# Kernel optimization log

Measured on AMD Instinct MI355X. Metric: run time of the kernel, lower is better.

The kernel has to match this reference:

```python
import jax, jax.numpy as jnp
import numpy as np


def segment_softmax(x, seg, num_segments):
    # numerically-stable softmax over graph segments (rows of the sparse matrix)
    m = jax.ops.segment_max(x, seg, num_segments=num_segments)
    e = jnp.exp(x - m[seg])
    s = jax.ops.segment_sum(e, seg, num_segments=num_segments)
    return e / s[seg]


def setup_inputs() -> dict:
    key = jax.random.key(0)
    ks = jax.random.split(key, 12)
    B, N, E, P, H = 256, 51200, 102400, 5, 300
    instruction = jax.random.normal(ks[0], (B, H), dtype=jnp.float32)
    distribution = jax.random.uniform(ks[1], (N,), dtype=jnp.float32)
    node_attrs = jax.random.normal(ks[2], (N, H), dtype=jnp.float32)
    edge_attrs = jax.random.normal(ks[3], (E, H), dtype=jnp.float32)
    node_indices = jnp.sort(jax.random.randint(ks[4], (N,), 0, B)).astype(jnp.int32)
    edge_batch_indices = jax.random.randint(ks[5], (E,), 0, B).astype(jnp.int32)
    edge_indices = jax.random.randint(ks[6], (2, E), 0, N).astype(jnp.int32)
    prop_embeds = jax.random.normal(ks[7], (P, H), dtype=jnp.float32)
    Ws_property = jax.random.uniform(ks[8], (P, H, H), dtype=jnp.float32)
    W_state = jax.random.uniform(ks[9], (H,), dtype=jnp.float32)
    W_relation = jax.random.uniform(ks[10], (H,), dtype=jnp.float32)
    return {"instruction": instruction, "distribution": distribution, "node_attrs": node_attrs,
            "edge_attrs": edge_attrs, "node_indices": node_indices,
            "edge_batch_indices": edge_batch_indices, "edge_indices": edge_indices,
            "prop_embeds": prop_embeds, "Ws_property": Ws_property,
            "W_state": W_state, "W_relation": W_relation}


def reference(instruction, distribution, node_attrs, edge_attrs, node_indices,
              edge_batch_indices, edge_indices, prop_embeds, Ws_property,
              W_state, W_relation):
    B = instruction.shape[0]
    # [B, P] property similarities
    prop_sim = jax.nn.softmax(instruction @ prop_embeds.T, axis=1)
    ps_node = prop_sim[node_indices]            # [N, P]
    instr_node = instruction[node_indices]      # [N, H]
    # per-property transform of node attrs: [N, P-1, H]
    wx = jnp.einsum('phk,nk->nph', Ws_property[:-1], node_attrs)
    node_scores = jax.nn.elu(jnp.sum(ps_node[:, :-1, None] * instr_node[:, None, :] * wx, axis=1))  # [N, H]
    # relation transform of edge attrs: [E, H]
    edge_wx = jnp.einsum('hk,ek->eh', Ws_property[-1], edge_attrs)
    edge_scores = jax.nn.elu(instruction[edge_batch_indices] * edge_wx)  # [E, H]
    # per-graph (segment) softmax over state logits
    state_logits = node_scores @ W_state        # [N]
    next_states = segment_softmax(state_logits, node_indices, B)
    # scatter-add message passing: dst node accumulates distribution[src] * edge_scores
    agg = jnp.zeros_like(node_scores).at[edge_indices[1]].add(
        distribution[edge_indices[0], None] * edge_scores)  # [N, H]
    rel_logits = agg @ W_relation               # [N]
    next_relations = segment_softmax(rel_logits, node_indices, B)
    r = ps_node[:, -1]
    next_distribution = r * next_relations + (1.0 - r) * next_states
    return next_distribution, prop_sim
```

## Files before the change

### kernel.cpp

```cpp
#include <hip/hip_runtime.h>
#include <math.h>

#define H 300
#define PP 5
#define NE 128
#define KC 32
#define NCH 10
#define ROWB 128
#define WTILE (320 * ROWB)
#define WHALF (160 * ROWB)
#define ATILE (NE * ROWB)
#define NTHREADS 256
#define GT 512

using short8 = __attribute__((ext_vector_type(8))) short;
using f32x4  = __attribute__((ext_vector_type(4))) float;

__device__ __forceinline__ float wsum64(float v) {
#pragma unroll
    for (int m = 32; m >= 1; m >>= 1) v += __shfl_xor(v, m, 64);
    return v;
}
__device__ __forceinline__ float wmax64(float v) {
#pragma unroll
    for (int m = 32; m >= 1; m >>= 1) v = fmaxf(v, __shfl_xor(v, m, 64));
    return v;
}
__device__ __forceinline__ float eluf(float x) { return x > 0.f ? x : expm1f(x); }

__device__ __forceinline__ unsigned short f2bf(float x) {
    unsigned int u = __float_as_uint(x);
    unsigned int r = u + 0x7FFF + ((u >> 16) & 1);
    return (unsigned short)(r >> 16);
}
__device__ __forceinline__ float bf2f(unsigned short h) {
    return __uint_as_float(((unsigned int)h) << 16);
}
__device__ __forceinline__ int sw(int r, int kb) {
    return r * ROWB + (kb ^ ((r & 7) << 4));
}
__device__ __forceinline__ void split4(const float* v, uint2& ph, uint2& pl) {
    unsigned short hs[4], ls[4];
#pragma unroll
    for (int i = 0; i < 4; ++i) {
        hs[i] = f2bf(v[i]);
        ls[i] = f2bf(v[i] - bf2f(hs[i]));
    }
    ph = make_uint2((unsigned)hs[0] | ((unsigned)hs[1] << 16),
                    (unsigned)hs[2] | ((unsigned)hs[3] << 16));
    pl = make_uint2((unsigned)ls[0] | ((unsigned)ls[1] << 16),
                    (unsigned)ls[2] | ((unsigned)ls[3] << 16));
}
__device__ __forceinline__ void gload16(const void* g, void* lds) {
    __builtin_amdgcn_global_load_lds(
        (const __attribute__((address_space(1))) unsigned int*)g,
        (__attribute__((address_space(3))) unsigned int*)lds, 16, 0, 0);
}
#define SBAR() __builtin_amdgcn_s_barrier()
#define SCHED() __builtin_amdgcn_sched_barrier(0)
#define WAIT_LGKM() asm volatile("s_waitcnt lgkmcnt(0)" ::: "memory")
#define WAIT_VM0()  asm volatile("s_waitcnt vmcnt(0)" ::: "memory")
#define WAIT_VM4()  asm volatile("s_waitcnt vmcnt(4)" ::: "memory")
#define WAIT_VM5()  asm volatile("s_waitcnt vmcnt(5)" ::: "memory")

__global__ void k_prop_sim(const float* __restrict__ instr,
                           const float* __restrict__ pe,
                           float* __restrict__ prop_sim) {
    int b = blockIdx.x, lane = threadIdx.x;
    float dots[PP];
#pragma unroll
    for (int p = 0; p < PP; ++p) {
        float s = 0.f;
        for (int hh = lane; hh < H; hh += 64) s += instr[b * H + hh] * pe[p * H + hh];
        dots[p] = wsum64(s);
    }
    if (lane == 0) {
        float m = dots[0];
#pragma unroll
        for (int p = 1; p < PP; ++p) m = fmaxf(m, dots[p]);
        float e[PP], s = 0.f;
#pragma unroll
        for (int p = 0; p < PP; ++p) { e[p] = expf(dots[p] - m); s += e[p]; }
        float inv = 1.f / s;
#pragma unroll
        for (int p = 0; p < PP; ++p) prop_sim[b * PP + p] = e[p] * inv;
    }
}

__global__ void k_counts(const int* __restrict__ idx, int* __restrict__ counts, int N) {
    int i = blockIdx.x * blockDim.x + threadIdx.x;
    if (i < N) atomicAdd(&counts[idx[i]], 1);
}

__global__ void k_scan(const int* __restrict__ counts, int* __restrict__ offsets, int B) {
    __shared__ int sh[256];
    int t = threadIdx.x;
    int c = (t < B) ? counts[t] : 0;
    sh[t] = c;
    __syncthreads();
    for (int off = 1; off < 256; off <<= 1) {
        int v = (t >= off) ? sh[t - off] : 0;
        __syncthreads();
        sh[t] += v;
        __syncthreads();
    }
    if (t < B) offsets[t] = sh[t] - c;
    if (t == B - 1) offsets[B] = sh[t];
}

__global__ void k_presplit(const float* __restrict__ W4, char* __restrict__ img) {
    int c = blockIdx.x;
    int idx = blockIdx.y * NTHREADS + threadIdx.x;
    int r = idx >> 3, j = idx & 7;
    int k = c * KC + j * 4;
    float v[4] = {0.f, 0.f, 0.f, 0.f};
    if (r < H && k < H) *(float4*)v = *(const float4*)&W4[(size_t)r * H + k];
    uint2 ph, pl;
    split4(v, ph, pl);
    char* row = img + (size_t)c * WTILE + (size_t)r * ROWB;
    int x = (r & 7) << 4;
    *(uint2*)(row + ((j * 8) ^ x)) = ph;
    *(uint2*)(row + ((64 + j * 8) ^ x)) = pl;
}

__global__ void k_combine(const float* __restrict__ Ws,
                          const float* __restrict__ prop_sim,
                          char* __restrict__ img) {
    int b = blockIdx.x, c = blockIdx.y, t = threadIdx.x;
    float ps0 = prop_sim[b * PP + 0], ps1 = prop_sim[b * PP + 1];
    float ps2 = prop_sim[b * PP + 2], ps3 = prop_sim[b * PP + 3];
    char* tile = img + ((size_t)b * NCH + c) * WTILE;
#pragma unroll
    for (int i = 0; i < 10; ++i) {
        int idx = t + i * NTHREADS;
        int r = idx >> 3, j = idx & 7;
        int k = c * KC + j * 4;
        float cv[4] = {0.f, 0.f, 0.f, 0.f};
        if (r < H && k < H) {
            size_t base = (size_t)r * H + k;
            float w0[4], w1[4], w2[4], w3[4];
            *(float4*)w0 = *(const float4*)&Ws[0 * (size_t)H * H + base];
            *(float4*)w1 = *(const float4*)&Ws[1 * (size_t)H * H + base];
            *(float4*)w2 = *(const float4*)&Ws[2 * (size_t)H * H + base];
            *(float4*)w3 = *(const float4*)&Ws[3 * (size_t)H * H + base];
#pragma unroll
            for (int q = 0; q < 4; ++q)
                cv[q] = fmaf(ps0, w0[q], fmaf(ps1, w1[q], fmaf(ps2, w2[q], ps3 * w3[q])));
        }
        uint2 ph, pl;
        split4(cv, ph, pl);
        char* row = tile + (size_t)r * ROWB;
        int x = (r & 7) << 4;
        *(uint2*)(row + ((j * 8) ^ x)) = ph;
        *(uint2*)(row + ((64 + j * 8) ^ x)) = pl;
    }
}

__global__ __launch_bounds__(GT, 2) void k_gemm(
    const float* __restrict__ na, const float* __restrict__ ea,
    const char* __restrict__ Wc_img, const char* __restrict__ Wr_img,
    const float* __restrict__ instr, const float* __restrict__ wstate,
    const float* __restrict__ wrel,
    const int* __restrict__ offsets, const int* __restrict__ eb,
    const int* __restrict__ ei, const float* __restrict__ dist,
    float* __restrict__ slog, float* __restrict__ rlog,
    int N, int E, int nodeBlks)
{
    __shared__ __align__(16) char W_t[2][WHALF];
    __shared__ __align__(16) char A_t[ATILE];

    int bid = blockIdx.x;
    int hz = blockIdx.y;
    bool isNode = bid < nodeBlks;
    const float* Asrc;
    const char* Wsrc;
    int base, rowmax, b = 0, nn = NE;
    if (isNode) {
        int low3 = bid & 7, q = bid >> 3;
        int tile = q % 3, bhi = q / 3;
        b = bhi * 8 + low3;
        int start = offsets[b], end = offsets[b + 1];
        base = start + tile * NE;
        if (base >= end) return;
        nn = min(NE, end - base);
        rowmax = N - 1;
        Asrc = na;
        Wsrc = Wc_img + (size_t)b * NCH * WTILE + (size_t)hz * WHALF;
    } else {
        base = (bid - nodeBlks) * NE;
        rowmax = E - 1;
        Asrc = ea;
        Wsrc = Wr_img + (size_t)hz * WHALF;
    }

    int t = threadIdx.x;
    int w = t >> 6, l = t & 63, lane16 = l & 15, g = l >> 4;
    int wn = w & 3, wh = w >> 2;

    f32x4 acc[5][2];
#pragma unroll
    for (int ht = 0; ht < 5; ++ht)
#pragma unroll
        for (int cg = 0; cg < 2; ++cg) acc[ht][cg] = (f32x4){0.f, 0.f, 0.f, 0.f};

    float4 pa[2];

    auto loadA = [&](int c) {
#pragma unroll
        for (int i = 0; i < 2; ++i) {
            int idx = t + i * GT;
            int r = idx >> 3, j = idx & 7;
            int k = c * KC + j * 4;
            float4 v = {0.f, 0.f, 0.f, 0.f};
            if (k < H) {
                int row = min(base + r, rowmax);
                v = *(const float4*)&Asrc[(size_t)row * H + k];
            }
            pa[i] = v;
        }
    };
    auto storeA = [&]() {
#pragma unroll
        for (int i = 0; i < 2; ++i) {
            int idx = t + i * GT;
            int r = idx >> 3, j = idx & 7;
            float v[4] = {pa[i].x, pa[i].y, pa[i].z, pa[i].w};
            uint2 ph, pl;
            split4(v, ph, pl);
            *(uint2*)(A_t + sw(r, j * 8)) = ph;
            *(uint2*)(A_t + sw(r, 64 + j * 8)) = pl;
        }
    };
    auto gloadW = [&](int c, int sel) {
        const char* src = Wsrc + (size_t)c * WTILE;
        char* dst = W_t[sel];
        int off = w * 1024 + (l << 4);
        gload16(src + off, dst + off);
        gload16(src + 8192 + off, dst + 8192 + off);
        if (w < 4) gload16(src + 16384 + off, dst + 16384 + off);
    };

    loadA(0);
    gloadW(0, 0);
    storeA();
    loadA(1);
    gloadW(1, 1);
    SCHED();
    if (w < 4) { WAIT_VM5(); } else { WAIT_VM4(); }
    WAIT_LGKM();
    SBAR();
    SCHED();

    int curb = 0;
    for (int c = 0; c < NCH; ++c) {
        short8 bh[2], bl[2];
#pragma unroll
        for (int cg = 0; cg < 2; ++cg) {
            int brow = wn * 32 + cg * 16 + lane16;
            bh[cg] = *(const short8*)(A_t + sw(brow, g * 16));
            bl[cg] = *(const short8*)(A_t + sw(brow, 64 + g * 16));
        }
#pragma unroll
        for (int ht = 0; ht < 5; ++ht) {
            int arow = wh * 80 + ht * 16 + lane16;
            short8 ah = *(const short8*)(W_t[curb] + sw(arow, g * 16));
            short8 al = *(const short8*)(W_t[curb] + sw(arow, 64 + g * 16));
#pragma unroll
            for (int cg = 0; cg < 2; ++cg) {
                acc[ht][cg] = __builtin_amdgcn_mfma_f32_16x16x32_bf16(ah, bh[cg], acc[ht][cg], 0, 0, 0);
                acc[ht][cg] = __builtin_amdgcn_mfma_f32_16x16x32_bf16(ah, bl[cg], acc[ht][cg], 0, 0, 0);
                acc[ht][cg] = __builtin_amdgcn_mfma_f32_16x16x32_bf16(al, bh[cg], acc[ht][cg], 0, 0, 0);
            }
        }
        if (c + 1 < NCH) {
            WAIT_LGKM();
            SBAR();
            SCHED();
            storeA();
            if (c + 2 < NCH) {
                loadA(c + 2);
                gloadW(c + 2, curb);
                SCHED();
                if (w < 4) { WAIT_VM5(); } else { WAIT_VM4(); }
            } else {
                SCHED();
                WAIT_VM0();
            }
            WAIT_LGKM();
            SBAR();
            SCHED();
            curb ^= 1;
        }
    }

    if (isNode) {
        const float* insb = instr + (size_t)b * H;
#pragma unroll
        for (int cg = 0; cg < 2; ++cg) {
            float part = 0.f;
#pragma unroll
            for (int ht = 0; ht < 5; ++ht) {
                int hb = hz * 160 + wh * 80 + ht * 16 + g * 4;
#pragma unroll
                for (int r = 0; r < 4; ++r) {
                    int h = hb + r;
                    if (h < H) part += wstate[h] * eluf(insb[h] * acc[ht][cg][r]);
                }
            }
            part += __shfl_xor(part, 16, 64);
            part += __shfl_xor(part, 32, 64);
            int col = wn * 32 + cg * 16 + lane16;
            if (l < 16 && col < nn) atomicAdd(&slog[base + col], part);
        }
    } else {
#pragma unroll
        for (int cg = 0; cg < 2; ++cg) {
            int e = base + wn * 32 + cg * 16 + lane16;
            int be = eb[e];
            const float* insb = instr + (size_t)be * H;
            float part = 0.f;
#pragma unroll
            for (int ht = 0; ht < 5; ++ht) {
                int hb = hz * 160 + wh * 80 + ht * 16 + g * 4;
#pragma unroll
                for (int r = 0; r < 4; ++r) {
                    int h = hb + r;
                    if (h < H) part += wrel[h] * eluf(insb[h] * acc[ht][cg][r]);
                }
            }
            part += __shfl_xor(part, 16, 64);
            part += __shfl_xor(part, 32, 64);
            if (l < 16) atomicAdd(&rlog[ei[E + e]], dist[ei[e]] * part);
        }
    }
}

__global__ void k_final(const float* __restrict__ slog, const float* __restrict__ rlog,
                        const float* __restrict__ prop_sim, const int* __restrict__ offsets,
                        float* __restrict__ out)
{
    int b = blockIdx.x;
    int s0 = offsets[b], e1 = offsets[b + 1];
    int t = threadIdx.x, wave = t >> 6, lane = t & 63;
    __shared__ float shA[4], shB[4];
    float mS = -3.0e38f, mR = -3.0e38f;
    for (int i = s0 + t; i < e1; i += 256) {
        mS = fmaxf(mS, slog[i]);
        mR = fmaxf(mR, rlog[i]);
    }
    mS = wmax64(mS); mR = wmax64(mR);
    if (lane == 0) { shA[wave] = mS; shB[wave] = mR; }
    __syncthreads();
    mS = fmaxf(fmaxf(shA[0], shA[1]), fmaxf(shA[2], shA[3]));
    mR = fmaxf(fmaxf(shB[0], shB[1]), fmaxf(shB[2], shB[3]));
    __syncthreads();
    float sS = 0.f, sR = 0.f;
    for (int i = s0 + t; i < e1; i += 256) {
        sS += expf(slog[i] - mS);
        sR += expf(rlog[i] - mR);
    }
    sS = wsum64(sS); sR = wsum64(sR);
    if (lane == 0) { shA[wave] = sS; shB[wave] = sR; }
    __syncthreads();
    sS = shA[0] + shA[1] + shA[2] + shA[3];
    sR = shB[0] + shB[1] + shB[2] + shB[3];
    float r = prop_sim[b * PP + (PP - 1)];
    float iS = 1.f / sS, iR = 1.f / sR;
    for (int i = s0 + t; i < e1; i += 256) {
        float ns = expf(slog[i] - mS) * iS;
        float nr = expf(rlog[i] - mR) * iR;
        out[i] = r * nr + (1.f - r) * ns;
    }
}

extern "C" void kernel_launch(void* const* d_in, const int* in_sizes, int n_in,
                              void* d_out, int out_size, void* d_ws, size_t ws_size,
                              hipStream_t stream) {
    (void)n_in; (void)out_size; (void)ws_size;
    const float* instruction  = (const float*)d_in[0];
    const float* distribution = (const float*)d_in[1];
    const float* node_attrs   = (const float*)d_in[2];
    const float* edge_attrs   = (const float*)d_in[3];
    const int*   node_indices = (const int*)d_in[4];
    const int*   edge_batch   = (const int*)d_in[5];
    const int*   edge_indices = (const int*)d_in[6];
    const float* prop_embeds  = (const float*)d_in[7];
    const float* Ws           = (const float*)d_in[8];
    const float* W_state      = (const float*)d_in[9];
    const float* W_rel        = (const float*)d_in[10];

    int B = in_sizes[0] / H;
    int N = in_sizes[1];
    int E = in_sizes[5];

    float* out = (float*)d_out;
    float* prop_sim = out + N;

    float* ws = (float*)d_ws;
    float* state_logits = ws;
    float* rel_logits   = ws + N;
    int*   offsets      = (int*)(ws + 2 * (size_t)N);
    int*   counts       = offsets + (B + 1);
    uintptr_t wsp = (uintptr_t)(counts + B);
    wsp = (wsp + 255) & ~(uintptr_t)255;
    char* Wr_img = (char*)wsp;
    char* Wc_img = Wr_img + (size_t)NCH * WTILE;

    size_t zero_bytes = (size_t)2 * N * sizeof(float) + (size_t)(2 * B + 1) * sizeof(int);
    hipMemsetAsync(d_ws, 0, zero_bytes, stream);

    int nodeBlks = 3 * B;
    int edgeBlks = E / NE;

    k_prop_sim<<<B, 64, 0, stream>>>(instruction, prop_embeds, prop_sim);
    k_presplit<<<dim3(NCH, 10), NTHREADS, 0, stream>>>(Ws + 4 * (size_t)H * H, Wr_img);
    k_counts<<<(N + 255) / 256, 256, 0, stream>>>(node_indices, counts, N);
    k_scan<<<1, 256, 0, stream>>>(counts, offsets, B);
    k_combine<<<dim3(B, NCH), NTHREADS, 0, stream>>>(Ws, prop_sim, Wc_img);
    k_gemm<<<dim3(nodeBlks + edgeBlks, 2), GT, 0, stream>>>(
        node_attrs, edge_attrs, Wc_img, Wr_img, instruction, W_state, W_rel,
        offsets, edge_batch, edge_indices, distribution,
        state_logits, rel_logits, N, E, nodeBlks);
    k_final<<<B, 256, 0, stream>>>(state_logits, rel_logits, prop_sim, offsets, out);
}
```

Before: 337.9 us.

## Fold instruction scaling into combined weights and interleave gemm grid order

The per-batch instruction vector is folded into the combined property weight image during k_combine, which removes the per-element instruction multiply from the node epilogue of the gemm. The gemm grid is flattened from 2D to 1D and remapped so both H-halves of the same tile and neighbouring batches run as adjacent blocks. This is meant to improve L2 reuse of the A tiles and weight images. The epilogue saving is small, and the remap changes the order in which the workgroups are scheduled.

```diff
diff --git a/kernel.cpp b/kernel.cpp
--- a/kernel.cpp
+++ b/kernel.cpp
@@ -125,6 +125,7 @@
 
 __global__ void k_combine(const float* __restrict__ Ws,
                           const float* __restrict__ prop_sim,
+                          const float* __restrict__ instr,
                           char* __restrict__ img) {
     int b = blockIdx.x, c = blockIdx.y, t = threadIdx.x;
     float ps0 = prop_sim[b * PP + 0], ps1 = prop_sim[b * PP + 1];
@@ -137,6 +138,7 @@
         int k = c * KC + j * 4;
         float cv[4] = {0.f, 0.f, 0.f, 0.f};
         if (r < H && k < H) {
+            float insv = instr[(size_t)b * H + r];
             size_t base = (size_t)r * H + k;
             float w0[4], w1[4], w2[4], w3[4];
             *(float4*)w0 = *(const float4*)&Ws[0 * (size_t)H * H + base];
@@ -145,7 +147,7 @@
             *(float4*)w3 = *(const float4*)&Ws[3 * (size_t)H * H + base];
 #pragma unroll
             for (int q = 0; q < 4; ++q)
-                cv[q] = fmaf(ps0, w0[q], fmaf(ps1, w1[q], fmaf(ps2, w2[q], ps3 * w3[q])));
+                cv[q] = insv * fmaf(ps0, w0[q], fmaf(ps1, w1[q], fmaf(ps2, w2[q], ps3 * w3[q])));
         }
         uint2 ph, pl;
         split4(cv, ph, pl);
@@ -164,21 +166,22 @@
     const int* __restrict__ offsets, const int* __restrict__ eb,
     const int* __restrict__ ei, const float* __restrict__ dist,
     float* __restrict__ slog, float* __restrict__ rlog,
-    int N, int E, int nodeBlks)
+    int N, int E, int nodeVX)
 {
     __shared__ __align__(16) char W_t[2][WHALF];
     __shared__ __align__(16) char A_t[ATILE];
 
-    int bid = blockIdx.x;
-    int hz = blockIdx.y;
-    bool isNode = bid < nodeBlks;
+    int x = blockIdx.x;
+    bool isNode = x < nodeVX;
     const float* Asrc;
     const char* Wsrc;
-    int base, rowmax, b = 0, nn = NE;
+    int base, rowmax, b = 0, hz, nn = NE;
     if (isNode) {
-        int low3 = bid & 7, q = bid >> 3;
-        int tile = q % 3, bhi = q / 3;
-        b = bhi * 8 + low3;
+        int gq = x / 48, r = x - gq * 48;
+        int k = r >> 3;
+        b = gq * 8 + (r & 7);
+        int tile = k >> 1;
+        hz = k & 1;
         int start = offsets[b], end = offsets[b + 1];
         base = start + tile * NE;
         if (base >= end) return;
@@ -187,7 +190,11 @@
         Asrc = na;
         Wsrc = Wc_img + (size_t)b * NCH * WTILE + (size_t)hz * WHALF;
     } else {
-        base = (bid - nodeBlks) * NE;
+        int y = x - nodeVX;
+        int gq = y / 16, r = y - gq * 16;
+        int e = gq * 8 + (r & 7);
+        hz = r >> 3;
+        base = e * NE;
         rowmax = E - 1;
         Asrc = ea;
         Wsrc = Wr_img + (size_t)hz * WHALF;
@@ -294,7 +301,6 @@
     }
 
     if (isNode) {
-        const float* insb = instr + (size_t)b * H;
 #pragma unroll
         for (int cg = 0; cg < 2; ++cg) {
             float part = 0.f;
@@ -304,7 +310,7 @@
 #pragma unroll
                 for (int r = 0; r < 4; ++r) {
                     int h = hb + r;
-                    if (h < H) part += wstate[h] * eluf(insb[h] * acc[ht][cg][r]);
+                    if (h < H) part += wstate[h] * eluf(acc[ht][cg][r]);
                 }
             }
             part += __shfl_xor(part, 16, 64);
@@ -409,17 +415,17 @@
     size_t zero_bytes = (size_t)2 * N * sizeof(float) + (size_t)(2 * B + 1) * sizeof(int);
     hipMemsetAsync(d_ws, 0, zero_bytes, stream);
 
-    int nodeBlks = 3 * B;
-    int edgeBlks = E / NE;
+    int nodeVX = 6 * B;
+    int edgeVX = (E / NE) * 2;
 
     k_prop_sim<<<B, 64, 0, stream>>>(instruction, prop_embeds, prop_sim);
     k_presplit<<<dim3(NCH, 10), NTHREADS, 0, stream>>>(Ws + 4 * (size_t)H * H, Wr_img);
     k_counts<<<(N + 255) / 256, 256, 0, stream>>>(node_indices, counts, N);
     k_scan<<<1, 256, 0, stream>>>(counts, offsets, B);
-    k_combine<<<dim3(B, NCH), NTHREADS, 0, stream>>>(Ws, prop_sim, Wc_img);
-    k_gemm<<<dim3(nodeBlks + edgeBlks, 2), GT, 0, stream>>>(
+    k_combine<<<dim3(B, NCH), NTHREADS, 0, stream>>>(Ws, prop_sim, instruction, Wc_img);
+    k_gemm<<<nodeVX + edgeVX, GT, 0, stream>>>(
         node_attrs, edge_attrs, Wc_img, Wr_img, instruction, W_state, W_rel,
         offsets, edge_batch, edge_indices, distribution,
-        state_logits, rel_logits, N, E, nodeBlks);
+        state_logits, rel_logits, N, E, nodeVX);
     k_final<<<B, 256, 0, stream>>>(state_logits, rel_logits, prop_sim, offsets, out);
 }
```

New measurement: 315.7 us. -6.6%, faster.
